# Kernel tuning notes

Measured on AMD Instinct MI355X. Metric: run time of the kernel, lower is better.

The kernel has to match this reference:

```python
import jax, jax.numpy as jnp
import numpy as np

BETA = 1.0
B, N, D = 2048, 131072, 256

def setup_inputs() -> dict:
    key = jax.random.key(0)
    k1, k2 = jax.random.split(key)
    x = jax.random.normal(k1, (B, D), dtype=jnp.float32)
    stored = jax.random.normal(k2, (N, D), dtype=jnp.float32)
    return {"x": x, "stored": stored}

def reference(x, stored):
    # scores: [B, N] = beta * x @ stored^T
    scores = BETA * jnp.einsum('bd,nd->bn', x, stored)
    attn = jax.nn.softmax(scores, axis=-1)
    # retrieved patterns: [B, D]
    return jnp.einsum('bn,nd->bd', attn, stored)
```

## Files before the change

### kernel.cpp

```cpp
#include <hip/hip_runtime.h>
#include <hip/hip_bf16.h>
#include <math.h>

#define B_Q 2048
#define N_K 131072
#define D_DIM 256
#define NCHUNK 32
#define CHUNK_KEYS (N_K / NCHUNK)
#define KTILE 32
#define NITER (CHUNK_KEYS / KTILE)
#define NTILES (N_K / KTILE)
#define TILE_USHORTS 16384
#define LOG2E 1.44269504f

typedef __attribute__((ext_vector_type(8))) _Float16 half8;
typedef __attribute__((ext_vector_type(8))) short bf16x8;
typedef __attribute__((ext_vector_type(4))) short bf16x4;
typedef __attribute__((ext_vector_type(2))) __fp16 fp16x2;
typedef __attribute__((ext_vector_type(4))) float f32x4;
typedef __attribute__((ext_vector_type(16))) float f32x16;

static __device__ __forceinline__ unsigned pkrtz(float a, float b) {
    fp16x2 h = __builtin_amdgcn_cvt_pkrtz(a, b);
    return __builtin_bit_cast(unsigned, h);
}
static __device__ __forceinline__ unsigned short f2bf(float f) {
    unsigned u = __builtin_bit_cast(unsigned, f);
    unsigned r = (u + 0x7fffu + ((u >> 16) & 1u)) >> 16;
    return (unsigned short)r;
}
static __device__ __forceinline__ unsigned cvt_pk_bf16(float lo, float hi) {
    unsigned d;
    asm("v_cvt_pk_bf16_f32 %0, %1, %2" : "=v"(d) : "v"(lo), "v"(hi));
    return d;
}

typedef const __attribute__((address_space(1))) unsigned int* gas_p;
typedef __attribute__((address_space(3))) unsigned int* las_p;
static __device__ __forceinline__ void gl_lds16(const void* g, void* l) {
    __builtin_amdgcn_global_load_lds((gas_p)g, (las_p)l, 16, 0, 0);
}

__global__ __launch_bounds__(512) void prepass(const float* __restrict__ stored,
                                               unsigned short* __restrict__ frag) {
    const int tid = threadIdx.x;
    const int t = blockIdx.x;
    const float* src = stored + (size_t)t * 32 * 256;
    unsigned short* out = frag + (size_t)t * TILE_USHORTS;
#pragma unroll
    for (int i = 0; i < 2; ++i) {
        int ck = i * 512 + tid;
        int l = ck & 63, s = ck >> 6;
        int key = l & 31, h = l >> 5;
        int d0 = s * 16 + h * 8;
        const float* p = src + key * 256 + d0;
        f32x4 a = *(const f32x4*)p;
        f32x4 b = *(const f32x4*)(p + 4);
        union { uint4 v; unsigned e[4]; } o;
        o.e[0] = pkrtz(a[0] * LOG2E, a[1] * LOG2E);
        o.e[1] = pkrtz(a[2] * LOG2E, a[3] * LOG2E);
        o.e[2] = pkrtz(b[0] * LOG2E, b[1] * LOG2E);
        o.e[3] = pkrtz(b[2] * LOG2E, b[3] * LOG2E);
        *(uint4*)(out + ck * 8) = o.v;
    }
#pragma unroll
    for (int i = 0; i < 2; ++i) {
        int cv = i * 512 + tid;
        int l = cv & 63, blkv = cv >> 6;
        int dn = blkv >> 1, ks = blkv & 1;
        int colv = l & 31, h = l >> 5;
        int d = dn * 32 + colv;
        int k0 = ks * 16 + h * 8;
        union { uint4 v; unsigned e[4]; } o;
#pragma unroll
        for (int j2 = 0; j2 < 4; ++j2) {
            float v0 = src[(k0 + 2 * j2) * 256 + d];
            float v1 = src[(k0 + 2 * j2 + 1) * 256 + d];
            o.e[j2] = cvt_pk_bf16(v0, v1);
        }
        *(uint4*)(out + 8192 + cv * 8) = o.v;
    }
}

__global__ __launch_bounds__(256, 2)
void hopfield_main(const float* __restrict__ x,
                   const unsigned short* __restrict__ frag,
                   unsigned short* __restrict__ partOb,
                   float* __restrict__ partl) {
    __shared__ __align__(16) unsigned short Kb[2][8192];
    __shared__ __align__(16) unsigned short Vb[2][8192];

    const int tid = threadIdx.x;
    const int wave = tid >> 6, lane = tid & 63;
    const int col = lane & 31, hf = lane >> 5;
    const int blk = blockIdx.x;
    const int chunk = blk & 31, qb = blk >> 5;
    const int q0w = qb * 128 + wave * 32;
    const unsigned short* fbase = frag + (size_t)chunk * NITER * TILE_USHORTS;

    half8 xf[16];
    float ss = 0.f;
    {
        const float* xr = x + (size_t)(q0w + col) * 256 + hf * 8;
#pragma unroll
        for (int s = 0; s < 16; ++s) {
            f32x4 a = *(const f32x4*)(xr + s * 16);
            f32x4 b = *(const f32x4*)(xr + s * 16 + 4);
            union { half8 v; _Float16 e[8]; } h;
#pragma unroll
            for (int j = 0; j < 4; ++j) {
                h.e[j] = (_Float16)a[j]; h.e[4 + j] = (_Float16)b[j];
                ss += a[j] * a[j] + b[j] * b[j];
            }
            xf[s] = h.v;
        }
    }
    ss += __shfl_xor(ss, 32);
    const float negM0L = -(4.9f * sqrtf(ss) * LOG2E);

    f32x16 O[8];
    const f32x16 z16 = {0.f,0.f,0.f,0.f,0.f,0.f,0.f,0.f,
                        0.f,0.f,0.f,0.f,0.f,0.f,0.f,0.f};
#pragma unroll
    for (int dn = 0; dn < 8; ++dn) O[dn] = z16;
    float lacc = 0.f;

#pragma unroll
    for (int j = 0; j < 4; ++j) {
        int off = (wave * 4 + j) * 512 + lane * 8;
        gl_lds16(fbase + off, &Kb[0][off]);
        gl_lds16(fbase + 8192 + off, &Vb[0][off]);
    }

#pragma unroll 1
    for (int it = 0; it < NITER; ++it) {
        __syncthreads();

        if (it + 1 < NITER) {
            const unsigned short* nbase = fbase + (size_t)(it + 1) * TILE_USHORTS;
#pragma unroll
            for (int j = 0; j < 4; ++j) {
                int off = (wave * 4 + j) * 512 + lane * 8;
                gl_lds16(nbase + off, &Kb[(it + 1) & 1][off]);
                gl_lds16(nbase + 8192 + off, &Vb[(it + 1) & 1][off]);
            }
        }

        const unsigned short* K = Kb[it & 1];
        const unsigned short* V = Vb[it & 1];

        f32x16 S;
#pragma unroll
        for (int r = 0; r < 16; ++r) S[r] = negM0L;
        __builtin_amdgcn_s_setprio(1);
#pragma unroll
        for (int s = 0; s < 16; ++s) {
            half8 af = *(const half8*)(K + (s * 64 + lane) * 8);
            S = __builtin_amdgcn_mfma_f32_32x32x16_f16(af, xf[s], S, 0, 0, 0);
        }
        __builtin_amdgcn_s_setprio(0);

        float p0[8];
#pragma unroll
        for (int r = 0; r < 8; ++r) p0[r] = __builtin_amdgcn_exp2f(S[r]);
        lacc += ((p0[0] + p0[1]) + (p0[2] + p0[3])) + ((p0[4] + p0[5]) + (p0[6] + p0[7]));
        unsigned w0 = cvt_pk_bf16(p0[0], p0[1]);
        unsigned w1 = cvt_pk_bf16(p0[2], p0[3]);
        unsigned w2 = cvt_pk_bf16(p0[4], p0[5]);
        unsigned w3 = cvt_pk_bf16(p0[6], p0[7]);
        asm volatile("v_permlane32_swap_b32 %0, %1" : "+v"(w0), "+v"(w2));
        asm volatile("v_permlane32_swap_b32 %0, %1" : "+v"(w1), "+v"(w3));
        union { bf16x8 v; unsigned u[4]; } A0;
        A0.u[0] = w0; A0.u[1] = w1; A0.u[2] = w2; A0.u[3] = w3;
        bf16x8 pa0 = A0.v;

        __builtin_amdgcn_s_setprio(1);
#pragma unroll
        for (int dn = 0; dn < 8; ++dn) {
            bf16x8 bv0 = *(const bf16x8*)(V + ((dn * 2 + 0) * 64 + lane) * 8);
            O[dn] = __builtin_amdgcn_mfma_f32_32x32x16_bf16(pa0, bv0, O[dn], 0, 0, 0);
        }
        __builtin_amdgcn_s_setprio(0);

        float p1[8];
#pragma unroll
        for (int r = 0; r < 8; ++r) p1[r] = __builtin_amdgcn_exp2f(S[8 + r]);
        lacc += ((p1[0] + p1[1]) + (p1[2] + p1[3])) + ((p1[4] + p1[5]) + (p1[6] + p1[7]));
        unsigned w4 = cvt_pk_bf16(p1[0], p1[1]);
        unsigned w5 = cvt_pk_bf16(p1[2], p1[3]);
        unsigned w6 = cvt_pk_bf16(p1[4], p1[5]);
        unsigned w7 = cvt_pk_bf16(p1[6], p1[7]);
        asm volatile("v_permlane32_swap_b32 %0, %1" : "+v"(w4), "+v"(w6));
        asm volatile("v_permlane32_swap_b32 %0, %1" : "+v"(w5), "+v"(w7));
        union { bf16x8 v; unsigned u[4]; } A1;
        A1.u[0] = w4; A1.u[1] = w5; A1.u[2] = w6; A1.u[3] = w7;
        bf16x8 pa1 = A1.v;

        __builtin_amdgcn_s_setprio(1);
#pragma unroll
        for (int dn = 0; dn < 8; ++dn) {
            bf16x8 bv1 = *(const bf16x8*)(V + ((dn * 2 + 1) * 64 + lane) * 8);
            O[dn] = __builtin_amdgcn_mfma_f32_32x32x16_bf16(pa1, bv1, O[dn], 0, 0, 0);
        }
        __builtin_amdgcn_s_setprio(0);
    }

    lacc += __shfl_xor(lacc, 32);
    if (lane < 32)
        partl[(size_t)chunk * B_Q + q0w + lane] = lacc;

#pragma unroll
    for (int dn = 0; dn < 8; ++dn)
#pragma unroll
        for (int r = 0; r < 16; ++r) {
            int qrow = (r & 3) + 8 * (r >> 2) + 4 * hf;
            partOb[((size_t)chunk * B_Q + q0w + qrow) * 256 + dn * 32 + col] = f2bf(O[dn][r]);
        }
}

__global__ __launch_bounds__(256) void combine_kernel(const unsigned short* __restrict__ partOb,
                                                      const float* __restrict__ partl,
                                                      float* __restrict__ out) {
    const int tid = threadIdx.x;
    const int ql = tid >> 6;
    const int q  = blockIdx.x * 4 + ql;
    const int d0 = (tid & 63) * 4;
    float L = 0.f;
#pragma unroll
    for (int c = 0; c < NCHUNK; ++c) L += partl[(size_t)c * B_Q + q];
    float acc[4] = {0.f, 0.f, 0.f, 0.f};
#pragma unroll 4
    for (int c = 0; c < NCHUNK; ++c) {
        bf16x4 v = *(const bf16x4*)(partOb + ((size_t)c * B_Q + q) * 256 + d0);
#pragma unroll
        for (int j = 0; j < 4; ++j) {
            unsigned u = (unsigned)(unsigned short)v[j] << 16;
            acc[j] += __builtin_bit_cast(float, u);
        }
    }
    const float invL = 1.f / L;
    f32x4 o = {acc[0] * invL, acc[1] * invL, acc[2] * invL, acc[3] * invL};
    *(f32x4*)(out + (size_t)q * 256 + d0) = o;
}

extern "C" void kernel_launch(void* const* d_in, const int* in_sizes, int n_in,
                              void* d_out, int out_size, void* d_ws, size_t ws_size,
                              hipStream_t stream) {
    const float* x      = (const float*)d_in[0];
    const float* stored = (const float*)d_in[1];
    float* out = (float*)d_out;

    char* wsb = (char*)d_ws;
    unsigned short* frag  = (unsigned short*)wsb;
    unsigned short* partOb = (unsigned short*)(wsb + (size_t)134217728);
    float* partl = (float*)(wsb + (size_t)134217728 + 33554432);

    prepass<<<NTILES, 512, 0, stream>>>(stored, frag);
    hopfield_main<<<512, 256, 0, stream>>>(x, frag, partOb, partl);
    combine_kernel<<<512, 256, 0, stream>>>(partOb, partl, out);
}
```

Baseline: 464.1 us.

## Fuse prepass, main, and combine into one persistent kernel with grid barriers

Replaces three kernel launches with a single persistent kernel of 512 blocks. Each block converts 8 key tiles, then all blocks meet at a software grid barrier, run the attention chunk, meet at a second barrier, and perform the combine. The aim is to remove launch gaps and per-kernel tail effects. It relies on all 512 blocks being co-resident (2 per CU at 256 CUs) to avoid deadlock, and the prepass now runs with fewer, larger blocks.

After: 697.6 us. 1.5x slower.

```diff
diff --git a/kernel.cpp b/kernel.cpp
--- a/kernel.cpp
+++ b/kernel.cpp
@@ -12,6 +12,7 @@
 #define NTILES (N_K / KTILE)
 #define TILE_USHORTS 16384
 #define LOG2E 1.44269504f
+#define NBLK 512
 
 typedef __attribute__((ext_vector_type(8))) _Float16 half8;
 typedef __attribute__((ext_vector_type(8))) short bf16x8;
@@ -41,206 +42,232 @@
     __builtin_amdgcn_global_load_lds((gas_p)g, (las_p)l, 16, 0, 0);
 }
 
-__global__ __launch_bounds__(512) void prepass(const float* __restrict__ stored,
-                                               unsigned short* __restrict__ frag) {
-    const int tid = threadIdx.x;
-    const int t = blockIdx.x;
-    const float* src = stored + (size_t)t * 32 * 256;
-    unsigned short* out = frag + (size_t)t * TILE_USHORTS;
-#pragma unroll
-    for (int i = 0; i < 2; ++i) {
-        int ck = i * 512 + tid;
-        int l = ck & 63, s = ck >> 6;
-        int key = l & 31, h = l >> 5;
-        int d0 = s * 16 + h * 8;
-        const float* p = src + key * 256 + d0;
-        f32x4 a = *(const f32x4*)p;
-        f32x4 b = *(const f32x4*)(p + 4);
-        union { uint4 v; unsigned e[4]; } o;
-        o.e[0] = pkrtz(a[0] * LOG2E, a[1] * LOG2E);
-        o.e[1] = pkrtz(a[2] * LOG2E, a[3] * LOG2E);
-        o.e[2] = pkrtz(b[0] * LOG2E, b[1] * LOG2E);
-        o.e[3] = pkrtz(b[2] * LOG2E, b[3] * LOG2E);
-        *(uint4*)(out + ck * 8) = o.v;
-    }
-#pragma unroll
-    for (int i = 0; i < 2; ++i) {
-        int cv = i * 512 + tid;
-        int l = cv & 63, blkv = cv >> 6;
-        int dn = blkv >> 1, ks = blkv & 1;
-        int colv = l & 31, h = l >> 5;
-        int d = dn * 32 + colv;
-        int k0 = ks * 16 + h * 8;
-        union { uint4 v; unsigned e[4]; } o;
-#pragma unroll
-        for (int j2 = 0; j2 < 4; ++j2) {
-            float v0 = src[(k0 + 2 * j2) * 256 + d];
-            float v1 = src[(k0 + 2 * j2 + 1) * 256 + d];
-            o.e[j2] = cvt_pk_bf16(v0, v1);
-        }
-        *(uint4*)(out + 8192 + cv * 8) = o.v;
-    }
+static __device__ __forceinline__ void grid_barrier(unsigned* bar) {
+    __syncthreads();
+    if (threadIdx.x == 0) {
+        __threadfence();
+        unsigned prev = __hip_atomic_fetch_add(&bar[0], 1u, __ATOMIC_ACQ_REL,
+                                               __HIP_MEMORY_SCOPE_AGENT);
+        if (prev == NBLK - 1) {
+            __hip_atomic_store(&bar[16], 1u, __ATOMIC_RELEASE,
+                               __HIP_MEMORY_SCOPE_AGENT);
+        } else {
+            while (__hip_atomic_load(&bar[16], __ATOMIC_ACQUIRE,
+                                     __HIP_MEMORY_SCOPE_AGENT) == 0u) {
+                __builtin_amdgcn_s_sleep(8);
+            }
+        }
+        __threadfence();
+    }
+    __syncthreads();
 }
 
 __global__ __launch_bounds__(256, 2)
-void hopfield_main(const float* __restrict__ x,
-                   const unsigned short* __restrict__ frag,
-                   unsigned short* __restrict__ partOb,
-                   float* __restrict__ partl) {
+void hopfield_fused(const float* __restrict__ x,
+                    const float* __restrict__ stored,
+                    unsigned short* __restrict__ frag,
+                    unsigned short* __restrict__ partOb,
+                    float* __restrict__ partl,
+                    float* __restrict__ out,
+                    unsigned* __restrict__ bars) {
     __shared__ __align__(16) unsigned short Kb[2][8192];
     __shared__ __align__(16) unsigned short Vb[2][8192];
 
     const int tid = threadIdx.x;
-    const int wave = tid >> 6, lane = tid & 63;
-    const int col = lane & 31, hf = lane >> 5;
     const int blk = blockIdx.x;
-    const int chunk = blk & 31, qb = blk >> 5;
-    const int q0w = qb * 128 + wave * 32;
-    const unsigned short* fbase = frag + (size_t)chunk * NITER * TILE_USHORTS;
-
-    half8 xf[16];
-    float ss = 0.f;
+
+#pragma unroll 1
+    for (int tt = 0; tt < 8; ++tt) {
+        const int t = blk * 8 + tt;
+        const float* src = stored + (size_t)t * 32 * 256;
+        unsigned short* outp = frag + (size_t)t * TILE_USHORTS;
+#pragma unroll
+        for (int i = 0; i < 4; ++i) {
+            int ck = i * 256 + tid;
+            int l = ck & 63, s = ck >> 6;
+            int key = l & 31, h = l >> 5;
+            int d0 = s * 16 + h * 8;
+            const float* p = src + key * 256 + d0;
+            f32x4 a = *(const f32x4*)p;
+            f32x4 b = *(const f32x4*)(p + 4);
+            union { uint4 v; unsigned e[4]; } o;
+            o.e[0] = pkrtz(a[0] * LOG2E, a[1] * LOG2E);
+            o.e[1] = pkrtz(a[2] * LOG2E, a[3] * LOG2E);
+            o.e[2] = pkrtz(b[0] * LOG2E, b[1] * LOG2E);
+            o.e[3] = pkrtz(b[2] * LOG2E, b[3] * LOG2E);
+            *(uint4*)(outp + ck * 8) = o.v;
+        }
+#pragma unroll
+        for (int i = 0; i < 4; ++i) {
+            int cv = i * 256 + tid;
+            int l = cv & 63, blkv = cv >> 6;
+            int dn = blkv >> 1, ks = blkv & 1;
+            int colv = l & 31, h = l >> 5;
+            int d = dn * 32 + colv;
+            int k0 = ks * 16 + h * 8;
+            union { uint4 v; unsigned e[4]; } o;
+#pragma unroll
+            for (int j2 = 0; j2 < 4; ++j2) {
+                float v0 = src[(k0 + 2 * j2) * 256 + d];
+                float v1 = src[(k0 + 2 * j2 + 1) * 256 + d];
+                o.e[j2] = cvt_pk_bf16(v0, v1);
+            }
+            *(uint4*)(outp + 8192 + cv * 8) = o.v;
+        }
+    }
+
+    grid_barrier(bars);
+
     {
-        const float* xr = x + (size_t)(q0w + col) * 256 + hf * 8;
-#pragma unroll
-        for (int s = 0; s < 16; ++s) {
-            f32x4 a = *(const f32x4*)(xr + s * 16);
-            f32x4 b = *(const f32x4*)(xr + s * 16 + 4);
-            union { half8 v; _Float16 e[8]; } h;
+        const int wave = tid >> 6, lane = tid & 63;
+        const int col = lane & 31, hf = lane >> 5;
+        const int chunk = blk & 31, qb = blk >> 5;
+        const int q0w = qb * 128 + wave * 32;
+        const unsigned short* fbase = frag + (size_t)chunk * NITER * TILE_USHORTS;
+
+        half8 xf[16];
+        float ss = 0.f;
+        {
+            const float* xr = x + (size_t)(q0w + col) * 256 + hf * 8;
+#pragma unroll
+            for (int s = 0; s < 16; ++s) {
+                f32x4 a = *(const f32x4*)(xr + s * 16);
+                f32x4 b = *(const f32x4*)(xr + s * 16 + 4);
+                union { half8 v; _Float16 e[8]; } h;
+#pragma unroll
+                for (int j = 0; j < 4; ++j) {
+                    h.e[j] = (_Float16)a[j]; h.e[4 + j] = (_Float16)b[j];
+                    ss += a[j] * a[j] + b[j] * b[j];
+                }
+                xf[s] = h.v;
+            }
+        }
+        ss += __shfl_xor(ss, 32);
+        const float negM0L = -(4.9f * sqrtf(ss) * LOG2E);
+
+        f32x16 O[8];
+        const f32x16 z16 = {0.f,0.f,0.f,0.f,0.f,0.f,0.f,0.f,
+                            0.f,0.f,0.f,0.f,0.f,0.f,0.f,0.f};
+#pragma unroll
+        for (int dn = 0; dn < 8; ++dn) O[dn] = z16;
+        float lacc = 0.f;
+
+#pragma unroll
+        for (int j = 0; j < 4; ++j) {
+            int off = (wave * 4 + j) * 512 + lane * 8;
+            gl_lds16(fbase + off, &Kb[0][off]);
+            gl_lds16(fbase + 8192 + off, &Vb[0][off]);
+        }
+
+#pragma unroll 1
+        for (int it = 0; it < NITER; ++it) {
+            __syncthreads();
+
+            if (it + 1 < NITER) {
+                const unsigned short* nbase = fbase + (size_t)(it + 1) * TILE_USHORTS;
+#pragma unroll
+                for (int j = 0; j < 4; ++j) {
+                    int off = (wave * 4 + j) * 512 + lane * 8;
+                    gl_lds16(nbase + off, &Kb[(it + 1) & 1][off]);
+                    gl_lds16(nbase + 8192 + off, &Vb[(it + 1) & 1][off]);
+                }
+            }
+
+            const unsigned short* K = Kb[it & 1];
+            const unsigned short* V = Vb[it & 1];
+
+            f32x16 S;
+#pragma unroll
+            for (int r = 0; r < 16; ++r) S[r] = negM0L;
+            __builtin_amdgcn_s_setprio(1);
+#pragma unroll
+            for (int s = 0; s < 16; ++s) {
+                half8 af = *(const half8*)(K + (s * 64 + lane) * 8);
+                S = __builtin_amdgcn_mfma_f32_32x32x16_f16(af, xf[s], S, 0, 0, 0);
+            }
+            __builtin_amdgcn_s_setprio(0);
+
+            float p0[8];
+#pragma unroll
+            for (int r = 0; r < 8; ++r) p0[r] = __builtin_amdgcn_exp2f(S[r]);
+            lacc += ((p0[0] + p0[1]) + (p0[2] + p0[3])) + ((p0[4] + p0[5]) + (p0[6] + p0[7]));
+            unsigned w0 = cvt_pk_bf16(p0[0], p0[1]);
+            unsigned w1 = cvt_pk_bf16(p0[2], p0[3]);
+            unsigned w2 = cvt_pk_bf16(p0[4], p0[5]);
+            unsigned w3 = cvt_pk_bf16(p0[6], p0[7]);
+            asm volatile("v_permlane32_swap_b32 %0, %1" : "+v"(w0), "+v"(w2));
+            asm volatile("v_permlane32_swap_b32 %0, %1" : "+v"(w1), "+v"(w3));
+            union { bf16x8 v; unsigned u[4]; } A0;
+            A0.u[0] = w0; A0.u[1] = w1; A0.u[2] = w2; A0.u[3] = w3;
+            bf16x8 pa0 = A0.v;
+
+            __builtin_amdgcn_s_setprio(1);
+#pragma unroll
+            for (int dn = 0; dn < 8; ++dn) {
+                bf16x8 bv0 = *(const bf16x8*)(V + ((dn * 2 + 0) * 64 + lane) * 8);
+                O[dn] = __builtin_amdgcn_mfma_f32_32x32x16_bf16(pa0, bv0, O[dn], 0, 0, 0);
+            }
+            __builtin_amdgcn_s_setprio(0);
+
+            float p1[8];
+#pragma unroll
+            for (int r = 0; r < 8; ++r) p1[r] = __builtin_amdgcn_exp2f(S[8 + r]);
+            lacc += ((p1[0] + p1[1]) + (p1[2] + p1[3])) + ((p1[4] + p1[5]) + (p1[6] + p1[7]));
+            unsigned w4 = cvt_pk_bf16(p1[0], p1[1]);
+            unsigned w5 = cvt_pk_bf16(p1[2], p1[3]);
+            unsigned w6 = cvt_pk_bf16(p1[4], p1[5]);
+            unsigned w7 = cvt_pk_bf16(p1[6], p1[7]);
+            asm volatile("v_permlane32_swap_b32 %0, %1" : "+v"(w4), "+v"(w6));
+            asm volatile("v_permlane32_swap_b32 %0, %1" : "+v"(w5), "+v"(w7));
+            union { bf16x8 v; unsigned u[4]; } A1;
+            A1.u[0] = w4; A1.u[1] = w5; A1.u[2] = w6; A1.u[3] = w7;
+            bf16x8 pa1 = A1.v;
+
+            __builtin_amdgcn_s_setprio(1);
+#pragma unroll
+            for (int dn = 0; dn < 8; ++dn) {
+                bf16x8 bv1 = *(const bf16x8*)(V + ((dn * 2 + 1) * 64 + lane) * 8);
+                O[dn] = __builtin_amdgcn_mfma_f32_32x32x16_bf16(pa1, bv1, O[dn], 0, 0, 0);
+            }
+            __builtin_amdgcn_s_setprio(0);
+        }
+
+        lacc += __shfl_xor(lacc, 32);
+        if (lane < 32)
+            partl[(size_t)chunk * B_Q + q0w + lane] = lacc;
+
+#pragma unroll
+        for (int dn = 0; dn < 8; ++dn)
+#pragma unroll
+            for (int r = 0; r < 16; ++r) {
+                int qrow = (r & 3) + 8 * (r >> 2) + 4 * hf;
+                partOb[((size_t)chunk * B_Q + q0w + qrow) * 256 + dn * 32 + col] = f2bf(O[dn][r]);
+            }
+    }
+
+    grid_barrier(bars + 64);
+
+    {
+        const int ql = tid >> 6;
+        const int q  = blk * 4 + ql;
+        const int d0 = (tid & 63) * 4;
+        float L = 0.f;
+#pragma unroll
+        for (int c = 0; c < NCHUNK; ++c) L += partl[(size_t)c * B_Q + q];
+        float acc[4] = {0.f, 0.f, 0.f, 0.f};
+#pragma unroll 4
+        for (int c = 0; c < NCHUNK; ++c) {
+            bf16x4 v = *(const bf16x4*)(partOb + ((size_t)c * B_Q + q) * 256 + d0);
 #pragma unroll
             for (int j = 0; j < 4; ++j) {
-                h.e[j] = (_Float16)a[j]; h.e[4 + j] = (_Float16)b[j];
-                ss += a[j] * a[j] + b[j] * b[j];
-            }
-            xf[s] = h.v;
-        }
-    }
-    ss += __shfl_xor(ss, 32);
-    const float negM0L = -(4.9f * sqrtf(ss) * LOG2E);
-
-    f32x16 O[8];
-    const f32x16 z16 = {0.f,0.f,0.f,0.f,0.f,0.f,0.f,0.f,
-                        0.f,0.f,0.f,0.f,0.f,0.f,0.f,0.f};
-#pragma unroll
-    for (int dn = 0; dn < 8; ++dn) O[dn] = z16;
-    float lacc = 0.f;
-
-#pragma unroll
-    for (int j = 0; j < 4; ++j) {
-        int off = (wave * 4 + j) * 512 + lane * 8;
-        gl_lds16(fbase + off, &Kb[0][off]);
-        gl_lds16(fbase + 8192 + off, &Vb[0][off]);
-    }
-
-#pragma unroll 1
-    for (int it = 0; it < NITER; ++it) {
-        __syncthreads();
-
-        if (it + 1 < NITER) {
-            const unsigned short* nbase = fbase + (size_t)(it + 1) * TILE_USHORTS;
-#pragma unroll
-            for (int j = 0; j < 4; ++j) {
-                int off = (wave * 4 + j) * 512 + lane * 8;
-                gl_lds16(nbase + off, &Kb[(it + 1) & 1][off]);
-                gl_lds16(nbase + 8192 + off, &Vb[(it + 1) & 1][off]);
-            }
-        }
-
-        const unsigned short* K = Kb[it & 1];
-        const unsigned short* V = Vb[it & 1];
-
-        f32x16 S;
-#pragma unroll
-        for (int r = 0; r < 16; ++r) S[r] = negM0L;
-        __builtin_amdgcn_s_setprio(1);
-#pragma unroll
-        for (int s = 0; s < 16; ++s) {
-            half8 af = *(const half8*)(K + (s * 64 + lane) * 8);
-            S = __builtin_amdgcn_mfma_f32_32x32x16_f16(af, xf[s], S, 0, 0, 0);
-        }
-        __builtin_amdgcn_s_setprio(0);
-
-        float p0[8];
-#pragma unroll
-        for (int r = 0; r < 8; ++r) p0[r] = __builtin_amdgcn_exp2f(S[r]);
-        lacc += ((p0[0] + p0[1]) + (p0[2] + p0[3])) + ((p0[4] + p0[5]) + (p0[6] + p0[7]));
-        unsigned w0 = cvt_pk_bf16(p0[0], p0[1]);
-        unsigned w1 = cvt_pk_bf16(p0[2], p0[3]);
-        unsigned w2 = cvt_pk_bf16(p0[4], p0[5]);
-        unsigned w3 = cvt_pk_bf16(p0[6], p0[7]);
-        asm volatile("v_permlane32_swap_b32 %0, %1" : "+v"(w0), "+v"(w2));
-        asm volatile("v_permlane32_swap_b32 %0, %1" : "+v"(w1), "+v"(w3));
-        union { bf16x8 v; unsigned u[4]; } A0;
-        A0.u[0] = w0; A0.u[1] = w1; A0.u[2] = w2; A0.u[3] = w3;
-        bf16x8 pa0 = A0.v;
-
-        __builtin_amdgcn_s_setprio(1);
-#pragma unroll
-        for (int dn = 0; dn < 8; ++dn) {
-            bf16x8 bv0 = *(const bf16x8*)(V + ((dn * 2 + 0) * 64 + lane) * 8);
-            O[dn] = __builtin_amdgcn_mfma_f32_32x32x16_bf16(pa0, bv0, O[dn], 0, 0, 0);
-        }
-        __builtin_amdgcn_s_setprio(0);
-
-        float p1[8];
-#pragma unroll
-        for (int r = 0; r < 8; ++r) p1[r] = __builtin_amdgcn_exp2f(S[8 + r]);
-        lacc += ((p1[0] + p1[1]) + (p1[2] + p1[3])) + ((p1[4] + p1[5]) + (p1[6] + p1[7]));
-        unsigned w4 = cvt_pk_bf16(p1[0], p1[1]);
-        unsigned w5 = cvt_pk_bf16(p1[2], p1[3]);
-        unsigned w6 = cvt_pk_bf16(p1[4], p1[5]);
-        unsigned w7 = cvt_pk_bf16(p1[6], p1[7]);
-        asm volatile("v_permlane32_swap_b32 %0, %1" : "+v"(w4), "+v"(w6));
-        asm volatile("v_permlane32_swap_b32 %0, %1" : "+v"(w5), "+v"(w7));
-        union { bf16x8 v; unsigned u[4]; } A1;
-        A1.u[0] = w4; A1.u[1] = w5; A1.u[2] = w6; A1.u[3] = w7;
-        bf16x8 pa1 = A1.v;
-
-        __builtin_amdgcn_s_setprio(1);
-#pragma unroll
-        for (int dn = 0; dn < 8; ++dn) {
-            bf16x8 bv1 = *(const bf16x8*)(V + ((dn * 2 + 1) * 64 + lane) * 8);
-            O[dn] = __builtin_amdgcn_mfma_f32_32x32x16_bf16(pa1, bv1, O[dn], 0, 0, 0);
-        }
-        __builtin_amdgcn_s_setprio(0);
-    }
-
-    lacc += __shfl_xor(lacc, 32);
-    if (lane < 32)
-        partl[(size_t)chunk * B_Q + q0w + lane] = lacc;
-
-#pragma unroll
-    for (int dn = 0; dn < 8; ++dn)
-#pragma unroll
-        for (int r = 0; r < 16; ++r) {
-            int qrow = (r & 3) + 8 * (r >> 2) + 4 * hf;
-            partOb[((size_t)chunk * B_Q + q0w + qrow) * 256 + dn * 32 + col] = f2bf(O[dn][r]);
-        }
-}
-
-__global__ __launch_bounds__(256) void combine_kernel(const unsigned short* __restrict__ partOb,
-                                                      const float* __restrict__ partl,
-                                                      float* __restrict__ out) {
-    const int tid = threadIdx.x;
-    const int ql = tid >> 6;
-    const int q  = blockIdx.x * 4 + ql;
-    const int d0 = (tid & 63) * 4;
-    float L = 0.f;
-#pragma unroll
-    for (int c = 0; c < NCHUNK; ++c) L += partl[(size_t)c * B_Q + q];
-    float acc[4] = {0.f, 0.f, 0.f, 0.f};
-#pragma unroll 4
-    for (int c = 0; c < NCHUNK; ++c) {
-        bf16x4 v = *(const bf16x4*)(partOb + ((size_t)c * B_Q + q) * 256 + d0);
-#pragma unroll
-        for (int j = 0; j < 4; ++j) {
-            unsigned u = (unsigned)(unsigned short)v[j] << 16;
-            acc[j] += __builtin_bit_cast(float, u);
-        }
-    }
-    const float invL = 1.f / L;
-    f32x4 o = {acc[0] * invL, acc[1] * invL, acc[2] * invL, acc[3] * invL};
-    *(f32x4*)(out + (size_t)q * 256 + d0) = o;
+                unsigned u = (unsigned)(unsigned short)v[j] << 16;
+                acc[j] += __builtin_bit_cast(float, u);
+            }
+        }
+        const float invL = 1.f / L;
+        f32x4 o = {acc[0] * invL, acc[1] * invL, acc[2] * invL, acc[3] * invL};
+        *(f32x4*)(out + (size_t)q * 256 + d0) = o;
+    }
 }
 
 extern "C" void kernel_launch(void* const* d_in, const int* in_sizes, int n_in,
@@ -251,11 +278,11 @@
     float* out = (float*)d_out;
 
     char* wsb = (char*)d_ws;
-    unsigned short* frag  = (unsigned short*)wsb;
+    unsigned short* frag   = (unsigned short*)wsb;
     unsigned short* partOb = (unsigned short*)(wsb + (size_t)134217728);
     float* partl = (float*)(wsb + (size_t)134217728 + 33554432);
-
-    prepass<<<NTILES, 512, 0, stream>>>(stored, frag);
-    hopfield_main<<<512, 256, 0, stream>>>(x, frag, partOb, partl);
-    combine_kernel<<<512, 256, 0, stream>>>(partOb, partl, out);
-}
+    unsigned* bars = (unsigned*)(wsb + (size_t)134217728 + 33554432 + 262144);
+
+    hipMemsetAsync(bars, 0, 512, stream);
+    hopfield_fused<<<NBLK, 256, 0, stream>>>(x, stored, frag, partOb, partl, out, bars);
+}
```
